# Kernel optimization log

Measured on AMD Instinct MI355X. Metric: run time of the kernel, lower is better.

The kernel has to match this reference:

```python
import jax, jax.numpy as jnp
import numpy as np

N_STATE, N_OBS, BATCH, T_LEN = 256, 128, 64, 1024
RICCATI_ITERS = 300


def _steady_state_gain(A, H, Q, R, iters=RICCATI_ITERS):
    """Riccati iteration for the steady-state Kalman gain (numpy, fp64)."""
    n = A.shape[0]
    I = np.eye(n)
    P = np.eye(n)
    for _ in range(iters):
        Pp = A @ P @ A.T + Q
        S = H @ Pp @ H.T + R
        K = np.linalg.solve(S, (Pp @ H.T).T).T
        P = (I - K @ H) @ Pp
    return K


def setup_inputs() -> dict:
    rng = np.random.default_rng(0)
    # Stable dynamics: scaled orthogonal matrix (spectral radius 0.95).
    M = rng.standard_normal((N_STATE, N_STATE))
    Qm, _ = np.linalg.qr(M)
    A = 0.95 * Qm
    H = rng.standard_normal((N_OBS, N_STATE)) / np.sqrt(N_STATE)
    Qc = 0.1 * np.eye(N_STATE)
    Rc = 0.1 * np.eye(N_OBS)
    K = _steady_state_gain(A, H, Qc, Rc)

    key = jax.random.key(0)
    y = jax.random.normal(key, (BATCH, T_LEN, N_OBS), dtype=jnp.float32)
    return {
        "y": y,
        "A": jnp.asarray(A, dtype=jnp.float32),
        "H": jnp.asarray(H, dtype=jnp.float32),
        "K": jnp.asarray(K, dtype=jnp.float32),
    }


def reference(y, A, H, K):
    """Steady-state Kalman filter: x_t = (I - K H) A x_{t-1} + K y_t.

    y: [B, T, n_obs] -> out: [B, T, n_state]
    """
    n = A.shape[0]
    I = jnp.eye(n, dtype=A.dtype)
    A_eff = (I - K @ H) @ A  # [n, n]

    x0 = y[:, 0] @ K.T  # [B, n]

    def step(x, yt):
        x = x @ A_eff.T + yt @ K.T  # [B, n]
        return x, x

    ys = jnp.swapaxes(y[:, 1:], 0, 1)  # [T-1, B, n_obs]
    _, xs = jax.lax.scan(step, x0, ys)  # xs: [T-1, B, n]
    out = jnp.concatenate([x0[:, None, :], jnp.swapaxes(xs, 0, 1)], axis=1)
    return out  # [B, T, n_state]
```

## Files before the change

### kernel.cpp

```cpp
#include <hip/hip_runtime.h>
#include <hip/hip_bf16.h>

#define NS 256
#define MO 128
#define BB 64
#define TT 1024

typedef short s16x8 __attribute__((ext_vector_type(8)));
typedef float f32x4 __attribute__((ext_vector_type(4)));
typedef unsigned int uint;
typedef unsigned short ushort;

__device__ __forceinline__ ushort f2bf(float x) {
    uint u = __float_as_uint(x);
    uint r = (u + 0x7fffu + ((u >> 16) & 1u)) >> 16;
    return (ushort)r;
}
__device__ __forceinline__ float bf2f(ushort h) { return __uint_as_float(((uint)h) << 16); }

__device__ __forceinline__ uint pkbf2(float a, float b) {
    __hip_bfloat162 h = __float22bfloat162_rn(make_float2(a, b));
    union { __hip_bfloat162 b2; uint u; } cv;
    cv.b2 = h;
    return cv.u;
}

__device__ __forceinline__ void conv8(float4 f0, float4 f1, s16x8& vh, s16x8& vl) {
    uint h0 = pkbf2(f0.x, f0.y), h1 = pkbf2(f0.z, f0.w);
    uint h2 = pkbf2(f1.x, f1.y), h3 = pkbf2(f1.z, f1.w);
    float r0 = f0.x - __uint_as_float(h0 << 16);
    float r1 = f0.y - __uint_as_float(h0 & 0xffff0000u);
    float r2 = f0.z - __uint_as_float(h1 << 16);
    float r3 = f0.w - __uint_as_float(h1 & 0xffff0000u);
    float r4 = f1.x - __uint_as_float(h2 << 16);
    float r5 = f1.y - __uint_as_float(h2 & 0xffff0000u);
    float r6 = f1.z - __uint_as_float(h3 << 16);
    float r7 = f1.w - __uint_as_float(h3 & 0xffff0000u);
    uint l0 = pkbf2(r0, r1), l1 = pkbf2(r2, r3);
    uint l2 = pkbf2(r4, r5), l3 = pkbf2(r6, r7);
    union { uint u[4]; s16x8 v; } ch, cl;
    ch.u[0] = h0; ch.u[1] = h1; ch.u[2] = h2; ch.u[3] = h3;
    cl.u[0] = l0; cl.u[1] = l1; cl.u[2] = l2; cl.u[3] = l3;
    vh = ch.v; vl = cl.v;
}

__device__ __forceinline__ f32x4 mfma16(s16x8 a, s16x8 b, f32x4 c) {
    return __builtin_amdgcn_mfma_f32_16x16x32_bf16(a, b, c, 0, 0, 0);
}


__global__ void kh_kernel(const float* __restrict__ K, const float* __restrict__ H,
                          float* __restrict__ KH,
                          ushort* __restrict__ kbh, ushort* __restrict__ kbl) {
    int i = blockIdx.x, j = threadIdx.x;
    __shared__ float kl[MO];
    if (j < MO) {
        float v = K[i * MO + j];
        kl[j] = v;
        ushort hi = f2bf(v);
        kbh[i * MO + j] = hi;
        kbl[i * MO + j] = f2bf(v - bf2f(hi));
    }
    __syncthreads();
    float acc = 0.f;
#pragma unroll 8
    for (int k = 0; k < MO; ++k) acc += kl[k] * H[k * NS + j];
    KH[i * NS + j] = acc;
}

__global__ void aeff_kernel(const float* __restrict__ A, const float* __restrict__ KH,
                            float* __restrict__ AE,
                            ushort* __restrict__ aeh, ushort* __restrict__ ael) {
    int i = blockIdx.x, j = threadIdx.x;
    __shared__ float khr[NS];
    khr[j] = KH[i * NS + j];
    __syncthreads();
    float acc = A[i * NS + j];
#pragma unroll 8
    for (int k = 0; k < NS; ++k) acc -= khr[k] * A[k * NS + j];
    AE[i * NS + j] = acc;
    ushort hi = f2bf(acc);
    aeh[i * NS + j] = hi;
    ael[i * NS + j] = f2bf(acc - bf2f(hi));
}

__global__ void matsq_kernel(const float* __restrict__ src, float* __restrict__ dst,
                             ushort* dh, ushort* dl) {
    int i = blockIdx.x, j = threadIdx.x;
    __shared__ float row[NS];
    row[j] = src[i * NS + j];
    __syncthreads();
    float acc = 0.f;
#pragma unroll 8
    for (int k = 0; k < NS; ++k) acc += row[k] * src[k * NS + j];
    dst[i * NS + j] = acc;
    if (dh) {
        ushort hi = f2bf(acc);
        dh[i * NS + j] = hi;
        dl[i * NS + j] = f2bf(acc - bf2f(hi));
    }
}


__launch_bounds__(512, 2)
__global__ void ugemm_kernel(const float* __restrict__ y, const ushort* __restrict__ kbh,
                             const ushort* __restrict__ kbl, float* __restrict__ U) {
    const int tid = threadIdx.x, blk = blockIdx.x;
    const int w = tid >> 6, l = tid & 63, lr = l & 15, lg = l >> 4;

    __shared__ float xe[16 * NS];

    s16x8 KBh[2][4], KBl[2][4];
#pragma unroll
    for (int t2 = 0; t2 < 2; ++t2) {
        int row = 16 * (2 * w + t2) + lr;
#pragma unroll
        for (int q = 0; q < 4; ++q) {
            int off = row * MO + 32 * q + 8 * lg;
            KBh[t2][q] = *(const s16x8*)(kbh + off);
            KBl[t2][q] = *(const s16x8*)(kbl + off);
        }
    }

#pragma unroll 1
    for (int it = 0; it < 8; ++it) {
        long row0 = ((long)blk * 8 + it) * 16;
        s16x8 Ah[4], Al[4];
#pragma unroll
        for (int q = 0; q < 4; ++q) {
            long off = (row0 + lr) * MO + 32 * q + 8 * lg;
            float4 f0 = *(const float4*)(y + off);
            float4 f1 = *(const float4*)(y + off + 4);
            conv8(f0, f1, Ah[q], Al[q]);
        }
        f32x4 acc0 = {0.f, 0.f, 0.f, 0.f};
        f32x4 acc1 = {0.f, 0.f, 0.f, 0.f};
#pragma unroll
        for (int q = 0; q < 4; ++q) {
            acc0 = mfma16(Ah[q], KBh[0][q], acc0);
            acc0 = mfma16(Al[q], KBh[0][q], acc0);
            acc0 = mfma16(Ah[q], KBl[0][q], acc0);
            acc1 = mfma16(Ah[q], KBh[1][q], acc1);
            acc1 = mfma16(Al[q], KBh[1][q], acc1);
            acc1 = mfma16(Ah[q], KBl[1][q], acc1);
        }
        const int col0 = 32 * w + lr, col1 = col0 + 16;
#pragma unroll
        for (int i = 0; i < 4; ++i) {
            int m = 4 * lg + i;
            xe[(m * NS + col0) ^ ((m & 7) << 2)] = acc0[i];
            xe[(m * NS + col1) ^ ((m & 7) << 2)] = acc1[i];
        }
        __syncthreads();
#pragma unroll
        for (int j = 0; j < 2; ++j) {
            int idx = j * 512 + tid;
            int r = idx >> 6;
            int wb = idx << 2;
            float4 v = *(const float4*)&xe[wb ^ ((r & 7) << 2)];
            *(float4*)(U + (row0 + r) * NS + (wb & 255)) = v;
        }
        __syncthreads();
    }
}


template <int MODE>
__launch_bounds__(512, 2)
__global__ void scan16_kernel(const ushort* __restrict__ mh, const ushort* __restrict__ ml,
                              const float* uf, const ushort* __restrict__ ub,
                              const ushort* __restrict__ cin, float* outf,
                              ushort* __restrict__ wbf, ushort* __restrict__ ebf) {
    constexpr int S = (MODE == 2) ? 15 : ((MODE == 3) ? 7 : 8);
    constexpr bool UF32 = (MODE == 0 || MODE == 4);
    const int tid = threadIdx.x, blk = blockIdx.x;
    const int w = tid >> 6, l = tid & 63, lr = l & 15, lg = l >> 4;

    __shared__ ushort xh_s[2][16 * NS];
    __shared__ ushort xl_s[2][16 * NS];

    s16x8 Bh[2][8], Bl[2][8];
#pragma unroll
    for (int t2 = 0; t2 < 2; ++t2) {
        int row = 16 * (2 * w + t2) + lr;
#pragma unroll
        for (int q = 0; q < 8; ++q) {
            int off = row * NS + 32 * q + 8 * lg;
            Bh[t2][q] = *(const s16x8*)(mh + off);
            Bl[t2][q] = *(const s16x8*)(ml + off);
        }
    }

    const int b0 = (blk & 3) * 16;
    const int cc = blk >> 2;

#pragma unroll
    for (int jj = 0; jj < 8; ++jj) {
        int idx = jj * 512 + tid;
        int m = idx >> 8, col = idx & 255;
        ushort hu = 0;
        if constexpr (MODE == 3) {
            hu = cin[((long)blk * 16 + m) * NS + col];
            wbf[((long)blk * 128 + 8 * m) * NS + col] = hu;
        } else if constexpr (MODE == 4) {
            hu = cin[((long)(b0 + m) * 128 + cc) * NS + col];
        } else if constexpr (MODE == 2) {
            wbf[((long)(blk * 16 + m) * 16) * NS + col] = 0;
        }
        int si = (m * NS + col) ^ ((m & 7) << 3);
        xh_s[0][si] = hu;
        xl_s[0][si] = 0;
    }

    const int st0 = 32 * w + 4 * lg;
    const int st1 = st0 + 16;

    long ubase;
    if constexpr (UF32) {
        ubase = ((long)(b0 + lr) * TT + cc * 8) * NS;
    } else if constexpr (MODE == 1 || MODE == 3) {
        ubase = ((long)blk * 128 + 8 * lr) * NS;
    } else {
        ubase = ((long)(blk * 16 + lr) * 16) * NS;
    }

    auto ldu = [&](long off) -> f32x4 {
        if constexpr (UF32) {
            float4 v = *(const float4*)(uf + off);
            return f32x4{v.x, v.y, v.z, v.w};
        } else {
            uint2 v = *(const uint2*)(ub + off);
            return f32x4{__uint_as_float(v.x << 16), __uint_as_float(v.x & 0xffff0000u),
                         __uint_as_float(v.y << 16), __uint_as_float(v.y & 0xffff0000u)};
        }
    };

    f32x4 up0 = ldu(ubase + st0);
    f32x4 up1 = ldu(ubase + st1);
    __syncthreads();

    for (int s = 0; s < S; ++s) {
        const int cur = s & 1, nxt = cur ^ 1;
        f32x4 acc0 = up0, acc1 = up1;

#pragma unroll
        for (int q = 0; q < 8; ++q) {
            int ridx = (lr * NS + 32 * q + 8 * lg) ^ ((lr & 7) << 3);
            s16x8 xh = *(const s16x8*)&xh_s[cur][ridx];
            s16x8 xl = *(const s16x8*)&xl_s[cur][ridx];
            acc0 = mfma16(Bh[0][q], xh, acc0);
            acc0 = mfma16(Bh[0][q], xl, acc0);
            acc0 = mfma16(Bl[0][q], xh, acc0);
            acc1 = mfma16(Bh[1][q], xh, acc1);
            acc1 = mfma16(Bh[1][q], xl, acc1);
            acc1 = mfma16(Bl[1][q], xh, acc1);
        }

        if (s + 1 < S) {
            up0 = ldu(ubase + (long)(s + 1) * NS + st0);
            up1 = ldu(ubase + (long)(s + 1) * NS + st1);
        }

        uint h01a = pkbf2(acc0[0], acc0[1]), h23a = pkbf2(acc0[2], acc0[3]);
        uint h01b = pkbf2(acc1[0], acc1[1]), h23b = pkbf2(acc1[2], acc1[3]);

        if constexpr (MODE == 2) {
            long wb = ((long)(blk * 16 + lr) * 16 + s + 1) * NS;
            *(uint2*)(wbf + wb + st0) = make_uint2(h01a, h23a);
            *(uint2*)(wbf + wb + st1) = make_uint2(h01b, h23b);
        } else if constexpr (MODE == 3) {
            long wb = ((long)blk * 128 + 8 * lr + s + 1) * NS;
            *(uint2*)(wbf + wb + st0) = make_uint2(h01a, h23a);
            *(uint2*)(wbf + wb + st1) = make_uint2(h01b, h23b);
        } else if constexpr (MODE == 4) {
            long ob = ((long)(b0 + lr) * TT + cc * 8 + s) * NS;
            *(f32x4*)(outf + ob + st0) = acc0;
            *(f32x4*)(outf + ob + st1) = acc1;
        } else if constexpr (MODE == 0) {
            if (s == S - 1) {
                long eb = ((long)(b0 + lr) * 128 + cc) * NS;
                *(uint2*)(ebf + eb + st0) = make_uint2(h01a, h23a);
                *(uint2*)(ebf + eb + st1) = make_uint2(h01b, h23b);
            }
        } else if constexpr (MODE == 1) {
            if (s == S - 1) {
                long eb = ((long)blk * 16 + lr) * NS;
                *(uint2*)(ebf + eb + st0) = make_uint2(h01a, h23a);
                *(uint2*)(ebf + eb + st1) = make_uint2(h01b, h23b);
            }
        }

        if (s + 1 < S) {
            float la0 = acc0[0] - __uint_as_float(h01a << 16);
            float la1 = acc0[1] - __uint_as_float(h01a & 0xffff0000u);
            float la2 = acc0[2] - __uint_as_float(h23a << 16);
            float la3 = acc0[3] - __uint_as_float(h23a & 0xffff0000u);
            float lb0 = acc1[0] - __uint_as_float(h01b << 16);
            float lb1 = acc1[1] - __uint_as_float(h01b & 0xffff0000u);
            float lb2 = acc1[2] - __uint_as_float(h23b << 16);
            float lb3 = acc1[3] - __uint_as_float(h23b & 0xffff0000u);
            int wi0 = lr * NS + (st0 ^ ((lr & 7) << 3));
            int wi1 = lr * NS + (st1 ^ ((lr & 7) << 3));
            *(uint2*)&xh_s[nxt][wi0] = make_uint2(h01a, h23a);
            *(uint2*)&xh_s[nxt][wi1] = make_uint2(h01b, h23b);
            *(uint2*)&xl_s[nxt][wi0] = make_uint2(pkbf2(la0, la1), pkbf2(la2, la3));
            *(uint2*)&xl_s[nxt][wi1] = make_uint2(pkbf2(lb0, lb1), pkbf2(lb2, lb3));
        }
        __syncthreads();
    }
}


extern "C" void kernel_launch(void* const* d_in, const int* in_sizes, int n_in,
                              void* d_out, int out_size, void* d_ws, size_t ws_size,
                              hipStream_t stream) {
    const float* y = (const float*)d_in[0];
    const float* A = (const float*)d_in[1];
    const float* H = (const float*)d_in[2];
    const float* K = (const float*)d_in[3];
    float* out = (float*)d_out;

    float* ws = (float*)d_ws;
    const long MAT = (long)NS * NS;
    float* KH = ws + 0 * MAT;
    float* AE = ws + 1 * MAT;
    float* Ta = ws + 2 * MAT;
    float* Tb = ws + 3 * MAT;
    float* M8 = ws + 4 * MAT;
    float* M64 = ws + 5 * MAT;
    ushort* aeh = (ushort*)(ws + 6 * MAT);
    ushort* ael = aeh + MAT;
    ushort* mh = (ushort*)(ws + 7 * MAT);
    ushort* ml = mh + MAT;
    ushort* m2h = (ushort*)(ws + 8 * MAT);
    ushort* m2l = m2h + MAT;
    ushort* kbh = (ushort*)(ws + 9 * MAT);
    ushort* kbl = kbh + (long)NS * MO;
    ushort* e_buf = (ushort*)(ws + 10 * MAT);
    ushort* cbuf = (ushort*)(ws + 26 * MAT);
    ushort* e2 = (ushort*)(ws + 42 * MAT);
    ushort* c2 = (ushort*)(ws + 44 * MAT);

    float* U = out;

    kh_kernel<<<NS, NS, 0, stream>>>(K, H, KH, kbh, kbl);
    aeff_kernel<<<NS, NS, 0, stream>>>(A, KH, AE, aeh, ael);
    matsq_kernel<<<NS, NS, 0, stream>>>(AE, Ta, nullptr, nullptr);
    matsq_kernel<<<NS, NS, 0, stream>>>(Ta, Tb, nullptr, nullptr);
    matsq_kernel<<<NS, NS, 0, stream>>>(Tb, M8, mh, ml);
    matsq_kernel<<<NS, NS, 0, stream>>>(M8, Ta, nullptr, nullptr);
    matsq_kernel<<<NS, NS, 0, stream>>>(Ta, Tb, nullptr, nullptr);
    matsq_kernel<<<NS, NS, 0, stream>>>(Tb, M64, m2h, m2l);

    ugemm_kernel<<<512, 512, 0, stream>>>(y, kbh, kbl, U);

    scan16_kernel<0><<<512, 512, 0, stream>>>(aeh, ael, U, nullptr, nullptr, nullptr, nullptr, e_buf);
    scan16_kernel<1><<<64, 512, 0, stream>>>(mh, ml, nullptr, e_buf, nullptr, nullptr, nullptr, e2);
    scan16_kernel<2><<<4, 512, 0, stream>>>(m2h, m2l, nullptr, e2, nullptr, nullptr, c2, nullptr);
    scan16_kernel<3><<<64, 512, 0, stream>>>(mh, ml, nullptr, e_buf, c2, nullptr, cbuf, nullptr);
    scan16_kernel<4><<<512, 512, 0, stream>>>(aeh, ael, U, nullptr, cbuf, out, nullptr, nullptr);
}
```

Before: 259.3 us.

## Fuse y@K^T input projection into scan kernels and merge KH/Aeff setup

Removes the separate ugemm kernel that wrote U = y K^T (64x1024x256 fp32) to global memory. Instead, scan modes 0 and 4 each recompute their per-step u directly from y using split-bf16 MFMA with K held in registers. It also merges kh and aeff into one kernel so KH never goes through global memory. This saves a large fp32 write and two reads of U, plus a launch, but computes the projection twice and uses more registers in the scan kernels.

Result: slower. 282.8 us (+9.0%).

```diff
diff --git a/kernel.cpp b/kernel.cpp
--- a/kernel.cpp
+++ b/kernel.cpp
@@ -49,11 +49,13 @@
 }
 
 
-__global__ void kh_kernel(const float* __restrict__ K, const float* __restrict__ H,
-                          float* __restrict__ KH,
-                          ushort* __restrict__ kbh, ushort* __restrict__ kbl) {
+__global__ void khaeff_kernel(const float* __restrict__ K, const float* __restrict__ H,
+                              const float* __restrict__ A, float* __restrict__ AE,
+                              ushort* __restrict__ kbh, ushort* __restrict__ kbl,
+                              ushort* __restrict__ aeh, ushort* __restrict__ ael) {
     int i = blockIdx.x, j = threadIdx.x;
     __shared__ float kl[MO];
+    __shared__ float khr[NS];
     if (j < MO) {
         float v = K[i * MO + j];
         kl[j] = v;
@@ -65,23 +67,15 @@
     float acc = 0.f;
 #pragma unroll 8
     for (int k = 0; k < MO; ++k) acc += kl[k] * H[k * NS + j];
-    KH[i * NS + j] = acc;
-}
-
-__global__ void aeff_kernel(const float* __restrict__ A, const float* __restrict__ KH,
-                            float* __restrict__ AE,
-                            ushort* __restrict__ aeh, ushort* __restrict__ ael) {
-    int i = blockIdx.x, j = threadIdx.x;
-    __shared__ float khr[NS];
-    khr[j] = KH[i * NS + j];
+    khr[j] = acc;
     __syncthreads();
-    float acc = A[i * NS + j];
+    float ae = A[i * NS + j];
 #pragma unroll 8
-    for (int k = 0; k < NS; ++k) acc -= khr[k] * A[k * NS + j];
-    AE[i * NS + j] = acc;
-    ushort hi = f2bf(acc);
+    for (int k = 0; k < NS; ++k) ae -= khr[k] * A[k * NS + j];
+    AE[i * NS + j] = ae;
+    ushort hi = f2bf(ae);
     aeh[i * NS + j] = hi;
-    ael[i * NS + j] = f2bf(acc - bf2f(hi));
+    ael[i * NS + j] = f2bf(ae - bf2f(hi));
 }
 
 __global__ void matsq_kernel(const float* __restrict__ src, float* __restrict__ dst,
@@ -102,77 +96,15 @@
 }
 
 
-__launch_bounds__(512, 2)
-__global__ void ugemm_kernel(const float* __restrict__ y, const ushort* __restrict__ kbh,
-                             const ushort* __restrict__ kbl, float* __restrict__ U) {
-    const int tid = threadIdx.x, blk = blockIdx.x;
-    const int w = tid >> 6, l = tid & 63, lr = l & 15, lg = l >> 4;
-
-    __shared__ float xe[16 * NS];
-
-    s16x8 KBh[2][4], KBl[2][4];
-#pragma unroll
-    for (int t2 = 0; t2 < 2; ++t2) {
-        int row = 16 * (2 * w + t2) + lr;
-#pragma unroll
-        for (int q = 0; q < 4; ++q) {
-            int off = row * MO + 32 * q + 8 * lg;
-            KBh[t2][q] = *(const s16x8*)(kbh + off);
-            KBl[t2][q] = *(const s16x8*)(kbl + off);
-        }
-    }
-
-#pragma unroll 1
-    for (int it = 0; it < 8; ++it) {
-        long row0 = ((long)blk * 8 + it) * 16;
-        s16x8 Ah[4], Al[4];
-#pragma unroll
-        for (int q = 0; q < 4; ++q) {
-            long off = (row0 + lr) * MO + 32 * q + 8 * lg;
-            float4 f0 = *(const float4*)(y + off);
-            float4 f1 = *(const float4*)(y + off + 4);
-            conv8(f0, f1, Ah[q], Al[q]);
-        }
-        f32x4 acc0 = {0.f, 0.f, 0.f, 0.f};
-        f32x4 acc1 = {0.f, 0.f, 0.f, 0.f};
-#pragma unroll
-        for (int q = 0; q < 4; ++q) {
-            acc0 = mfma16(Ah[q], KBh[0][q], acc0);
-            acc0 = mfma16(Al[q], KBh[0][q], acc0);
-            acc0 = mfma16(Ah[q], KBl[0][q], acc0);
-            acc1 = mfma16(Ah[q], KBh[1][q], acc1);
-            acc1 = mfma16(Al[q], KBh[1][q], acc1);
-            acc1 = mfma16(Ah[q], KBl[1][q], acc1);
-        }
-        const int col0 = 32 * w + lr, col1 = col0 + 16;
-#pragma unroll
-        for (int i = 0; i < 4; ++i) {
-            int m = 4 * lg + i;
-            xe[(m * NS + col0) ^ ((m & 7) << 2)] = acc0[i];
-            xe[(m * NS + col1) ^ ((m & 7) << 2)] = acc1[i];
-        }
-        __syncthreads();
-#pragma unroll
-        for (int j = 0; j < 2; ++j) {
-            int idx = j * 512 + tid;
-            int r = idx >> 6;
-            int wb = idx << 2;
-            float4 v = *(const float4*)&xe[wb ^ ((r & 7) << 2)];
-            *(float4*)(U + (row0 + r) * NS + (wb & 255)) = v;
-        }
-        __syncthreads();
-    }
-}
-
-
 template <int MODE>
 __launch_bounds__(512, 2)
 __global__ void scan16_kernel(const ushort* __restrict__ mh, const ushort* __restrict__ ml,
-                              const float* uf, const ushort* __restrict__ ub,
+                              const ushort* __restrict__ kah, const ushort* __restrict__ kal,
+                              const float* __restrict__ y_g, const ushort* __restrict__ ub,
                               const ushort* __restrict__ cin, float* outf,
                               ushort* __restrict__ wbf, ushort* __restrict__ ebf) {
     constexpr int S = (MODE == 2) ? 15 : ((MODE == 3) ? 7 : 8);
-    constexpr bool UF32 = (MODE == 0 || MODE == 4);
+    constexpr bool YF = (MODE == 0 || MODE == 4);
     const int tid = threadIdx.x, blk = blockIdx.x;
     const int w = tid >> 6, l = tid & 63, lr = l & 15, lg = l >> 4;
 
@@ -188,6 +120,20 @@
             int off = row * NS + 32 * q + 8 * lg;
             Bh[t2][q] = *(const s16x8*)(mh + off);
             Bl[t2][q] = *(const s16x8*)(ml + off);
+        }
+    }
+
+    s16x8 KAh[2][4], KAl[2][4];
+    if constexpr (YF) {
+#pragma unroll
+        for (int t2 = 0; t2 < 2; ++t2) {
+            int row = 16 * (2 * w + t2) + lr;
+#pragma unroll
+            for (int q = 0; q < 4; ++q) {
+                int off = row * MO + 32 * q + 8 * lg;
+                KAh[t2][q] = *(const s16x8*)(kah + off);
+                KAl[t2][q] = *(const s16x8*)(kal + off);
+            }
         }
     }
 
@@ -215,9 +161,9 @@
     const int st0 = 32 * w + 4 * lg;
     const int st1 = st0 + 16;
 
-    long ubase;
-    if constexpr (UF32) {
-        ubase = ((long)(b0 + lr) * TT + cc * 8) * NS;
+    long ybase = 0, ubase = 0;
+    if constexpr (YF) {
+        ybase = ((long)(b0 + lr) * TT + cc * 8) * MO + 8 * lg;
     } else if constexpr (MODE == 1 || MODE == 3) {
         ubase = ((long)blk * 128 + 8 * lr) * NS;
     } else {
@@ -225,18 +171,37 @@
     }
 
     auto ldu = [&](long off) -> f32x4 {
-        if constexpr (UF32) {
-            float4 v = *(const float4*)(uf + off);
-            return f32x4{v.x, v.y, v.z, v.w};
-        } else {
-            uint2 v = *(const uint2*)(ub + off);
-            return f32x4{__uint_as_float(v.x << 16), __uint_as_float(v.x & 0xffff0000u),
-                         __uint_as_float(v.y << 16), __uint_as_float(v.y & 0xffff0000u)};
-        }
+        uint2 v = *(const uint2*)(ub + off);
+        return f32x4{__uint_as_float(v.x << 16), __uint_as_float(v.x & 0xffff0000u),
+                     __uint_as_float(v.y << 16), __uint_as_float(v.y & 0xffff0000u)};
     };
 
-    f32x4 up0 = ldu(ubase + st0);
-    f32x4 up1 = ldu(ubase + st1);
+    auto compute_u = [&](int s, f32x4& ua0, f32x4& ua1) {
+        ua0 = f32x4{0.f, 0.f, 0.f, 0.f};
+        ua1 = f32x4{0.f, 0.f, 0.f, 0.f};
+#pragma unroll
+        for (int q = 0; q < 4; ++q) {
+            long off = ybase + (long)s * MO + 32 * q;
+            float4 f0 = *(const float4*)(y_g + off);
+            float4 f1 = *(const float4*)(y_g + off + 4);
+            s16x8 yh, yl;
+            conv8(f0, f1, yh, yl);
+            ua0 = mfma16(KAh[0][q], yh, ua0);
+            ua0 = mfma16(KAl[0][q], yh, ua0);
+            ua0 = mfma16(KAh[0][q], yl, ua0);
+            ua1 = mfma16(KAh[1][q], yh, ua1);
+            ua1 = mfma16(KAl[1][q], yh, ua1);
+            ua1 = mfma16(KAh[1][q], yl, ua1);
+        }
+    };
+
+    f32x4 up0, up1;
+    if constexpr (YF) {
+        compute_u(0, up0, up1);
+    } else {
+        up0 = ldu(ubase + st0);
+        up1 = ldu(ubase + st1);
+    }
     __syncthreads();
 
     for (int s = 0; s < S; ++s) {
@@ -257,8 +222,12 @@
         }
 
         if (s + 1 < S) {
-            up0 = ldu(ubase + (long)(s + 1) * NS + st0);
-            up1 = ldu(ubase + (long)(s + 1) * NS + st1);
+            if constexpr (YF) {
+                compute_u(s + 1, up0, up1);
+            } else {
+                up0 = ldu(ubase + (long)(s + 1) * NS + st0);
+                up1 = ldu(ubase + (long)(s + 1) * NS + st1);
+            }
         }
 
         uint h01a = pkbf2(acc0[0], acc0[1]), h23a = pkbf2(acc0[2], acc0[3]);
@@ -322,29 +291,25 @@
 
     float* ws = (float*)d_ws;
     const long MAT = (long)NS * NS;
-    float* KH = ws + 0 * MAT;
-    float* AE = ws + 1 * MAT;
-    float* Ta = ws + 2 * MAT;
-    float* Tb = ws + 3 * MAT;
-    float* M8 = ws + 4 * MAT;
-    float* M64 = ws + 5 * MAT;
-    ushort* aeh = (ushort*)(ws + 6 * MAT);
+    float* AE = ws + 0 * MAT;
+    float* Ta = ws + 1 * MAT;
+    float* Tb = ws + 2 * MAT;
+    float* M8 = ws + 3 * MAT;
+    float* M64 = ws + 4 * MAT;
+    ushort* aeh = (ushort*)(ws + 5 * MAT);
     ushort* ael = aeh + MAT;
-    ushort* mh = (ushort*)(ws + 7 * MAT);
+    ushort* mh = (ushort*)(ws + 6 * MAT);
     ushort* ml = mh + MAT;
-    ushort* m2h = (ushort*)(ws + 8 * MAT);
+    ushort* m2h = (ushort*)(ws + 7 * MAT);
     ushort* m2l = m2h + MAT;
-    ushort* kbh = (ushort*)(ws + 9 * MAT);
+    ushort* kbh = (ushort*)(ws + 8 * MAT);
     ushort* kbl = kbh + (long)NS * MO;
-    ushort* e_buf = (ushort*)(ws + 10 * MAT);
-    ushort* cbuf = (ushort*)(ws + 26 * MAT);
-    ushort* e2 = (ushort*)(ws + 42 * MAT);
-    ushort* c2 = (ushort*)(ws + 44 * MAT);
-
-    float* U = out;
-
-    kh_kernel<<<NS, NS, 0, stream>>>(K, H, KH, kbh, kbl);
-    aeff_kernel<<<NS, NS, 0, stream>>>(A, KH, AE, aeh, ael);
+    ushort* e_buf = (ushort*)(ws + 9 * MAT);
+    ushort* cbuf = (ushort*)(ws + 25 * MAT);
+    ushort* e2 = (ushort*)(ws + 41 * MAT);
+    ushort* c2 = (ushort*)(ws + 43 * MAT);
+
+    khaeff_kernel<<<NS, NS, 0, stream>>>(K, H, A, AE, kbh, kbl, aeh, ael);
     matsq_kernel<<<NS, NS, 0, stream>>>(AE, Ta, nullptr, nullptr);
     matsq_kernel<<<NS, NS, 0, stream>>>(Ta, Tb, nullptr, nullptr);
     matsq_kernel<<<NS, NS, 0, stream>>>(Tb, M8, mh, ml);
@@ -352,11 +317,9 @@
     matsq_kernel<<<NS, NS, 0, stream>>>(Ta, Tb, nullptr, nullptr);
     matsq_kernel<<<NS, NS, 0, stream>>>(Tb, M64, m2h, m2l);
 
-    ugemm_kernel<<<512, 512, 0, stream>>>(y, kbh, kbl, U);
-
-    scan16_kernel<0><<<512, 512, 0, stream>>>(aeh, ael, U, nullptr, nullptr, nullptr, nullptr, e_buf);
-    scan16_kernel<1><<<64, 512, 0, stream>>>(mh, ml, nullptr, e_buf, nullptr, nullptr, nullptr, e2);
-    scan16_kernel<2><<<4, 512, 0, stream>>>(m2h, m2l, nullptr, e2, nullptr, nullptr, c2, nullptr);
-    scan16_kernel<3><<<64, 512, 0, stream>>>(mh, ml, nullptr, e_buf, c2, nullptr, cbuf, nullptr);
-    scan16_kernel<4><<<512, 512, 0, stream>>>(aeh, ael, U, nullptr, cbuf, out, nullptr, nullptr);
-}
+    scan16_kernel<0><<<512, 512, 0, stream>>>(aeh, ael, kbh, kbl, y, nullptr, nullptr, nullptr, nullptr, e_buf);
+    scan16_kernel<1><<<64, 512, 0, stream>>>(mh, ml, nullptr, nullptr, nullptr, e_buf, nullptr, nullptr, nullptr, e2);
+    scan16_kernel<2><<<4, 512, 0, stream>>>(m2h, m2l, nullptr, nullptr, nullptr, e2, nullptr, nullptr, c2, nullptr);
+    scan16_kernel<3><<<64, 512, 0, stream>>>(mh, ml, nullptr, nullptr, nullptr, e_buf, c2, nullptr, cbuf, nullptr);
+    scan16_kernel<4><<<512, 512, 0, stream>>>(aeh, ael, kbh, kbl, y, nullptr, cbuf, out, nullptr, nullptr);
+}
```
